# Kernel tuning notes

Hardware: AMD Instinct MI355X
Metric: run time of the kernel (lower is better)

The kernel has to match this reference:

```python
import jax, jax.numpy as jnp
import numpy as np

B, S, D_IN = 2, 2048, 2048
NUM_HEADS, NUM_KV_GROUPS, HEAD_DIM = 32, 8, 64
GROUP_SIZE = NUM_HEADS // NUM_KV_GROUPS  # 4
D_OUT = NUM_HEADS * HEAD_DIM  # 2048


def setup_inputs() -> dict:
    key = jax.random.key(0)
    k1, k2, k3, k4, k5 = jax.random.split(key, 5)
    scale_in = 1.0 / np.sqrt(D_IN)
    scale_out = 1.0 / np.sqrt(D_OUT)
    return {
        "x": jax.random.normal(k1, (B, S, D_IN), dtype=jnp.float32),
        # Linear weights stored torch-style as (out_features, in_features); y = x @ W.T
        "Wq": jax.random.uniform(k2, (D_OUT, D_IN), minval=-scale_in, maxval=scale_in, dtype=jnp.float32),
        "Wk": jax.random.uniform(k3, (NUM_KV_GROUPS * HEAD_DIM, D_IN), minval=-scale_in, maxval=scale_in, dtype=jnp.float32),
        "Wv": jax.random.uniform(k4, (NUM_KV_GROUPS * HEAD_DIM, D_IN), minval=-scale_in, maxval=scale_in, dtype=jnp.float32),
        "Wo": jax.random.uniform(k5, (D_IN, D_OUT), minval=-scale_out, maxval=scale_out, dtype=jnp.float32),
    }


def reference(x, Wq, Wk, Wv, Wo):
    b, s, _ = x.shape
    # Projections
    q = (x @ Wq.T).reshape(b, s, NUM_KV_GROUPS, GROUP_SIZE, HEAD_DIM)  # [b,s,g,r,d]
    k = (x @ Wk.T).reshape(b, s, NUM_KV_GROUPS, HEAD_DIM)              # [b,s,g,d]
    v = (x @ Wv.T).reshape(b, s, NUM_KV_GROUPS, HEAD_DIM)
    # Scores: broadcast each KV group over its group of query heads
    # (equivalent to repeat_interleave of K/V along head dim)
    scores = jnp.einsum("bqgrd,bkgd->bgrqk", q, k) / np.sqrt(HEAD_DIM).astype(jnp.float32)
    causal = jnp.tril(jnp.ones((s, s), dtype=bool))  # True = keep
    scores = jnp.where(causal, scores, jnp.finfo(scores.dtype).min)
    attn = jax.nn.softmax(scores, axis=-1)  # [b,g,r,q,k]
    ctx = jnp.einsum("bgrqk,bkgd->bqgrd", attn, v).reshape(b, s, D_OUT)
    out = ctx @ Wo.T
    # new_kv_cache (un-expanded keys/values, layout [b, g, s, d])
    keys = k.transpose(0, 2, 1, 3)
    values = v.transpose(0, 2, 1, 3)
    return out, (keys, values)
```

## Files before the change

kernel.cpp:

```cpp
#include <hip/hip_runtime.h>


#define B_   2
#define S_   2048
#define DIN  2048
#define NH   32
#define NKV  8
#define HD   64
#define DOUT 2048
#define NQKV 3072

#define QSCALE 0.18033688f

typedef short bf16x8 __attribute__((ext_vector_type(8)));
typedef short bf16x4 __attribute__((ext_vector_type(4)));
typedef float f32x4  __attribute__((ext_vector_type(4)));

__device__ __forceinline__ unsigned short f2bf(float f) {
  unsigned int u = __float_as_uint(f);
  u += 0x7fff + ((u >> 16) & 1);
  return (unsigned short)(u >> 16);
}

__device__ __forceinline__ f32x4 mfma16(bf16x4 a, bf16x4 b, f32x4 c) {
#if __has_builtin(__builtin_amdgcn_mfma_f32_16x16x16bf16_1k)
  return __builtin_amdgcn_mfma_f32_16x16x16bf16_1k(a, b, c, 0, 0, 0);
#else
  asm volatile("v_mfma_f32_16x16x16_bf16 %0, %1, %2, %0" : "+v"(c) : "v"(a), "v"(b));
  return c;
#endif
}

__device__ __forceinline__ void gld_lds16(const void* gptr, void* lptr) {
  __builtin_amdgcn_global_load_lds(
      (const __attribute__((address_space(1))) unsigned int*)gptr,
      (__attribute__((address_space(3))) unsigned int*)lptr,
      16, 0, 0);
}

__device__ __forceinline__ bf16x8 ds_read128(const unsigned short* p) {
  bf16x8 r;
  asm volatile("ds_read_b128 %0, %1"
               : "=v"(r)
               : "v"((const __attribute__((address_space(3))) unsigned short*)p));
  return r;
}

#define BAR() __builtin_amdgcn_s_barrier()
#define SB()  __builtin_amdgcn_sched_barrier(0)
#define VMCNT(n) asm volatile("s_waitcnt vmcnt(" #n ")")
#define LGKM0()                                   \
  do {                                            \
    asm volatile("s_waitcnt lgkmcnt(0)");         \
    __builtin_amdgcn_sched_barrier(0);            \
  } while (0)

__global__ __launch_bounds__(256) void cvt_all(
    const float* __restrict__ x,  const float* __restrict__ Wq,
    const float* __restrict__ Wk, const float* __restrict__ Wv,
    const float* __restrict__ Wo,
    unsigned short* __restrict__ xbf, unsigned short* __restrict__ wqkv,
    unsigned short* __restrict__ wobf) {
  int i = blockIdx.x * blockDim.x + threadIdx.x;
  const float* src; unsigned short* dst; int off;
  if (i < 2097152)      { src = x;  dst = xbf;                  off = i; }
  else if (i < 3145728) { src = Wq; dst = wqkv;                 off = i - 2097152; }
  else if (i < 3407872) { src = Wk; dst = wqkv + 2048 * 2048;   off = i - 3145728; }
  else if (i < 3670016) { src = Wv; dst = wqkv + 2560 * 2048;   off = i - 3407872; }
  else                  { src = Wo; dst = wobf;                 off = i - 3670016; }
  float4 f = ((const float4*)src)[off];
  ushort4 o;
  o.x = f2bf(f.x); o.y = f2bf(f.y); o.z = f2bf(f.z); o.w = f2bf(f.w);
  ((ushort4*)dst)[off] = o;
}

#define MMA_PHASE(MH, NHH, BF)                                                  \
  do {                                                                          \
    __builtin_amdgcn_s_setprio(1);                                              \
    _Pragma("unroll")                                                           \
    for (int kk = 0; kk < 2; ++kk)                                              \
      _Pragma("unroll")                                                         \
      for (int mr = 0; mr < 4; ++mr)                                            \
        _Pragma("unroll")                                                       \
        for (int nr = 0; nr < NR; ++nr)                                         \
          acc[(MH) * 4 + mr][(NHH) * NR + nr] =                                 \
              __builtin_amdgcn_mfma_f32_16x16x32_bf16(                          \
                  af[mr][kk], BF[nr][kk], acc[(MH) * 4 + mr][(NHH) * NR + nr],  \
                  0, 0, 0);                                                     \
    __builtin_amdgcn_s_setprio(0);                                              \
  } while (0)

#define WAITW()                                   \
  do {                                            \
    if constexpr (BN == 256) VMCNT(6);            \
    else                     VMCNT(4);            \
  } while (0)

template <int MODE, int BN, int NTN>
__global__ __launch_bounds__(512, 2) void gemm8p(
    const unsigned short* __restrict__ A,
    const unsigned short* __restrict__ Bm,
    int K,
    unsigned short* __restrict__ qbf,
    unsigned short* __restrict__ kbf,
    unsigned short* __restrict__ vtbf,
    float* __restrict__ kout,
    float* __restrict__ vout,
    float* __restrict__ cout) {
  constexpr int NR = BN / 128;
  constexpr int BHROW = BN / 2;
  __shared__ unsigned short As[2][256 * 64];
  __shared__ unsigned short Bs[2][BN * 64];

  const int tid  = threadIdx.x;
  const int lane = tid & 63;
  const int wave = tid >> 6;
  const int wm   = wave >> 2;
  const int wn   = wave & 3;
  const int quad = lane >> 4;
  const int r16  = lane & 15;

  const int NT = K / 64;

  const int nwg = gridDim.x;
  const int id  = blockIdx.x;
  const int sid = (id & 7) * (nwg >> 3) + (id >> 3);
  const int by  = sid / NTN;
  const int bx  = sid % NTN;
  const int aRowBase = by * 256;
  const int bColBase = bx * BN;

  f32x4 zero = {0.f, 0.f, 0.f, 0.f};
  f32x4 acc[8][2 * NR];
#pragma unroll
  for (int i = 0; i < 8; ++i)
#pragma unroll
    for (int j = 0; j < 2 * NR; ++j) acc[i][j] = zero;

  auto stageA = [&](int dbuf, int h, int t) {
    const int tt = t < NT ? t : NT - 1;
    const int k0 = tt * 64;
#pragma unroll
    for (int i = 0; i < 2; ++i) {
      const int chunk = (i * 8 + wave) * 64 + lane;
      const int row = chunk >> 3;
      const int slot = chunk & 7;
      const int gc = (slot ^ (row & 7)) * 8;
      gld_lds16(A + (size_t)(aRowBase + h * 128 + row) * K + k0 + gc,
                &As[dbuf][h * 8192 + (i * 8 + wave) * 512]);
    }
  };
  auto stageB = [&](int dbuf, int h, int t) {
    const int tt = t < NT ? t : NT - 1;
    const int k0 = tt * 64;
    if constexpr (BN == 256) {
#pragma unroll
      for (int i = 0; i < 2; ++i) {
        const int chunk = (i * 8 + wave) * 64 + lane;
        const int row = chunk >> 3;
        const int slot = chunk & 7;
        const int gc = (slot ^ (row & 7)) * 8;
        gld_lds16(Bm + (size_t)(bColBase + h * 128 + row) * K + k0 + gc,
                  &Bs[dbuf][h * 8192 + (i * 8 + wave) * 512]);
      }
    } else {
      const int chunk = wave * 64 + lane;
      const int row = chunk >> 3;
      const int slot = chunk & 7;
      const int gc = (slot ^ (row & 7)) * 8;
      gld_lds16(Bm + (size_t)(bColBase + h * 64 + row) * K + k0 + gc,
                &Bs[dbuf][h * 4096 + wave * 512]);
    }
  };

  bf16x8 af[4][2];
  bf16x8 b0[NR][2];
  bf16x8 b1[NR][2];

  auto readA = [&](int sbuf, int mh) {
#pragma unroll
    for (int mr = 0; mr < 4; ++mr)
#pragma unroll
      for (int kk = 0; kk < 2; ++kk) {
        const int row = mh * 128 + wm * 64 + mr * 16 + r16;
        const int slot = (kk * 4 + quad) ^ (r16 & 7);
        af[mr][kk] = ds_read128(&As[sbuf][row * 64 + slot * 8]);
      }
  };
  auto readB = [&](int sbuf, int nh, bf16x8 (&bf)[NR][2]) {
#pragma unroll
    for (int nr = 0; nr < NR; ++nr)
#pragma unroll
      for (int kk = 0; kk < 2; ++kk) {
        const int row = nh * BHROW + wn * (BN / 8) + nr * 16 + r16;
        const int slot = (kk * 4 + quad) ^ (r16 & 7);
        bf[nr][kk] = ds_read128(&Bs[sbuf][row * 64 + slot * 8]);
      }
  };

  stageA(0, 0, 0);
  stageB(0, 0, 0);
  stageB(0, 1, 0);
  stageA(0, 1, 0);
  stageA(1, 0, 1);
  stageB(1, 0, 1);
  stageB(1, 1, 1);
  WAITW();
  BAR(); SB();

  const int NIT = NT / 2;
  for (int i = 0; i < NIT; ++i) {
    const int e2 = 2 * i + 2, o2 = 2 * i + 3;

    readA(0, 0); readB(0, 0, b0);
    stageA(1, 1, 2 * i + 1);
    BAR();
    LGKM0();
    MMA_PHASE(0, 0, b0);
    BAR(); SB();

    readB(0, 1, b1);
    stageA(0, 0, e2);
    BAR();
    LGKM0();
    MMA_PHASE(0, 1, b1);
    BAR(); SB();

    readA(0, 1);
    stageB(0, 0, e2);
    BAR();
    LGKM0();
    MMA_PHASE(1, 0, b0);
    BAR(); SB();

    stageB(0, 1, e2);
    BAR();
    MMA_PHASE(1, 1, b1);
    WAITW();
    BAR(); SB();

    readA(1, 0); readB(1, 0, b0);
    stageA(0, 1, e2);
    BAR();
    LGKM0();
    MMA_PHASE(0, 0, b0);
    BAR(); SB();

    readB(1, 1, b1);
    stageA(1, 0, o2);
    BAR();
    LGKM0();
    MMA_PHASE(0, 1, b1);
    BAR(); SB();

    readA(1, 1);
    stageB(1, 0, o2);
    BAR();
    LGKM0();
    MMA_PHASE(1, 0, b0);
    BAR(); SB();

    stageB(1, 1, o2);
    BAR();
    MMA_PHASE(1, 1, b1);
    WAITW();
    BAR(); SB();
  }
  VMCNT(0);

#pragma unroll
  for (int mi = 0; mi < 8; ++mi) {
    const int mh = mi >> 2, mr = mi & 3;
#pragma unroll
    for (int ni = 0; ni < 2 * NR; ++ni) {
      const int nh = ni / NR, nr = ni % NR;
      const int rowb = aRowBase + mh * 128 + wm * 64 + mr * 16 + quad * 4;
      const int col  = bColBase +
                       (BN == 256 ? nh * 128 + wn * 32 + nr * 16
                                  : nh * 64 + wn * 16) + r16;
#pragma unroll
      for (int reg = 0; reg < 4; ++reg) {
        const float v = acc[mi][ni][reg];
        const int m = rowb + reg;
        if (MODE == 1) {
          cout[(size_t)m * DOUT + col] = v;
        } else {
          if (col < 2048) {
            qbf[(size_t)m * DOUT + col] = f2bf(v * QSCALE);
          } else if (col < 2560) {
            const int gg = (col - 2048) >> 6, d = col & 63;
            const int b = m >> 11, s = m & 2047;
            const size_t idx = ((size_t)(b * NKV + gg) * S_ + s) * HD + d;
            kbf[idx]  = f2bf(v);
            kout[idx] = v;
          } else {
            const int gg = (col - 2560) >> 6, d = col & 63;
            const int b = m >> 11, s = m & 2047;
            vtbf[((size_t)(b * NKV + gg) * HD + d) * S_ + s]  = f2bf(v);
            vout[((size_t)(b * NKV + gg) * S_ + s) * HD + d] = v;
          }
        }
      }
    }
  }
}

__global__ __launch_bounds__(512, 4) void attn_kernel(
    const unsigned short* __restrict__ Q,
    const unsigned short* __restrict__ Kb,
    const unsigned short* __restrict__ VT,
    unsigned short* __restrict__ ctx) {
  __shared__ unsigned short Kbuf[2][4096];
  __shared__ unsigned short Vbuf[2][4096];

  const int tid  = threadIdx.x;
  const int lane = tid & 63;
  const int wave = tid >> 6;
  const int grp  = wave >> 2;
  const int hw   = wave & 3;
  const int quad = lane >> 4;
  const int r16  = lane & 15;
  const int g    = blockIdx.y;
  const int b    = blockIdx.z;
  const int h    = g * 4 + hw;
  const int pairI = blockIdx.x;
  const int q0     = grp ? pairI * 32 : (63 - pairI) * 32;
  const int nT_own = grp ? pairI / 2 + 1 : (63 - pairI) / 2 + 1;
  const int nTa    = (63 - pairI) / 2 + 1;

  const unsigned short* Kh  = Kb + (size_t)(b * NKV + g) * S_ * HD;
  const unsigned short* VTh = VT + (size_t)(b * NKV + g) * HD * S_;

  const int srow   = lane >> 3;
  const int schunk = (lane & 7) ^ srow;

  bf16x8 aq[2][2];
#pragma unroll
  for (int mt = 0; mt < 2; ++mt)
#pragma unroll
    for (int kk = 0; kk < 2; ++kk)
      aq[mt][kk] = *(const bf16x8*)(Q + (size_t)(b * S_ + q0 + mt * 16 + r16) * DOUT +
                                    h * HD + kk * 32 + quad * 8);

  bf16x4 ones4;
#pragma unroll
  for (int i = 0; i < 4; ++i) ones4[i] = (short)0x3F80;

  f32x4 zero = {0.f, 0.f, 0.f, 0.f};
  f32x4 o[2][4];
  f32x4 l[2];
#pragma unroll
  for (int mt = 0; mt < 2; ++mt) {
    l[mt] = zero;
#pragma unroll
    for (int dt = 0; dt < 4; ++dt) o[mt][dt] = zero;
  }

  auto stage = [&](int buf, int kt) {
    const int kbase = kt * 64;
    gld_lds16(Kh + (size_t)(kbase + wave * 8 + srow) * HD + schunk * 8,
              &Kbuf[buf][wave * 512]);
    gld_lds16(VTh + (size_t)(wave * 8 + srow) * S_ + kbase + schunk * 8,
              &Vbuf[buf][wave * 512]);
  };

  stage(0, 0);
  __syncthreads();

  for (int kt = 0; kt < nTa; ++kt) {
    const int buf = kt & 1;
    if (kt + 1 < nTa) stage(buf ^ 1, kt + 1);

    if (kt < nT_own) {
      bf16x8 bk[4][2];
#pragma unroll
      for (int nt = 0; nt < 4; ++nt)
#pragma unroll
        for (int kk = 0; kk < 2; ++kk) {
          const int seg = nt * 2 + (r16 >> 3), r = r16 & 7;
          const int slot = (kk * 4 + quad) ^ r;
          bk[nt][kk] = *(const bf16x8*)&Kbuf[buf][seg * 512 + r * 64 + slot * 8];
        }

      const bool last = (kt == nT_own - 1);
#pragma unroll
      for (int mt = 0; mt < 2; ++mt) {
        f32x4 st[4];
#pragma unroll
        for (int nt = 0; nt < 4; ++nt) st[nt] = zero;
#pragma unroll
        for (int kk = 0; kk < 2; ++kk)
#pragma unroll
          for (int nt = 0; nt < 4; ++nt)
            st[nt] = __builtin_amdgcn_mfma_f32_16x16x32_bf16(bk[nt][kk], aq[mt][kk], st[nt], 0, 0, 0);

        bf16x4 pf[4];
#pragma unroll
        for (int nt = 0; nt < 4; ++nt) {
#pragma unroll
          for (int r = 0; r < 4; ++r) {
            float s = st[nt][r];
            if (last) {
              const int key = kt * 64 + nt * 16 + quad * 4 + r;
              const int row = q0 + mt * 16 + r16;
              if (key > row) s = -1e38f;
            }
            const float p = __builtin_amdgcn_exp2f(s);
            pf[nt][r] = (short)(__float_as_uint(p) >> 16);
          }
        }
#pragma unroll
        for (int nt = 0; nt < 4; ++nt) l[mt] = mfma16(pf[nt], ones4, l[mt]);
#pragma unroll
        for (int dt = 0; dt < 4; ++dt) {
          const int seg = dt * 2 + (r16 >> 3), r = r16 & 7;
#pragma unroll
          for (int nt = 0; nt < 4; ++nt) {
            const int slot = (nt * 2 + (quad >> 1)) ^ r;
            bf16x4 bv = *(const bf16x4*)&Vbuf[buf][seg * 512 + r * 64 + slot * 8 + (quad & 1) * 4];
            o[mt][dt] = mfma16(pf[nt], bv, o[mt][dt]);
          }
        }
      }
    }

    __syncthreads();
  }

#pragma unroll
  for (int mt = 0; mt < 2; ++mt) {
    f32x4 rl;
#pragma unroll
    for (int r = 0; r < 4; ++r) rl[r] = __builtin_amdgcn_rcpf(l[mt][r]);
#pragma unroll
    for (int dt = 0; dt < 4; ++dt)
#pragma unroll
      for (int r = 0; r < 4; ++r) {
        const int qq = q0 + mt * 16 + quad * 4 + r;
        ctx[(size_t)(b * S_ + qq) * DOUT + h * HD + dt * 16 + r16] =
            f2bf(o[mt][dt][r] * rl[r]);
      }
  }
}

extern "C" void kernel_launch(void* const* d_in, const int* in_sizes, int n_in,
                              void* d_out, int out_size, void* d_ws, size_t ws_size,
                              hipStream_t stream) {
  const float* x  = (const float*)d_in[0];
  const float* Wq = (const float*)d_in[1];
  const float* Wk = (const float*)d_in[2];
  const float* Wv = (const float*)d_in[3];
  const float* Wo = (const float*)d_in[4];

  float* out  = (float*)d_out;
  float* keys = out + (size_t)B_ * S_ * DOUT;
  float* vals = keys + (size_t)B_ * NKV * S_ * HD;

  unsigned short* xbf  = (unsigned short*)d_ws;
  unsigned short* wqkv = xbf  + (size_t)B_ * S_ * DIN;
  unsigned short* wobf = wqkv + (size_t)NQKV * DIN;
  unsigned short* qbf  = wobf + (size_t)DIN * DOUT;
  unsigned short* kbf  = qbf  + (size_t)B_ * S_ * DOUT;
  unsigned short* vtbf = kbf  + (size_t)B_ * NKV * S_ * HD;
  unsigned short* ctx  = vtbf + (size_t)B_ * NKV * S_ * HD;

  cvt_all<<<dim3(4718592 / 256), dim3(256), 0, stream>>>(x, Wq, Wk, Wv, Wo,
                                                         xbf, wqkv, wobf);

  gemm8p<0, 256, 12><<<dim3(192), dim3(512), 0, stream>>>(
      xbf, wqkv, DIN, qbf, kbf, vtbf, keys, vals, nullptr);

  attn_kernel<<<dim3(32, NKV, B_), dim3(512), 0, stream>>>(qbf, kbf, vtbf, ctx);

  gemm8p<1, 128, 16><<<dim3(256), dim3(512), 0, stream>>>(
      ctx, wobf, DOUT, nullptr, nullptr, nullptr, nullptr, nullptr, out);
}
```

Baseline: 295.6 us.

## Double-buffer A fragments and prefetch LDS reads ahead of MFMA phases

Splits the A-fragment registers into two sets and reorders the GEMM main loop so the LDS reads for the next MFMA phase are issued before the current phase's MFMAs run. This hides LDS read latency behind matrix work instead of waiting on it. The global-load wait points move earlier, with smaller vmcnt thresholds, and the loop prologue now preloads the first fragments. The extra fragment registers raise register pressure under the 512x2 launch bounds, and the retuned barrier and wait placement risks exposing global-load latency.

```diff
diff --git a/kernel.cpp b/kernel.cpp
--- a/kernel.cpp
+++ b/kernel.cpp
@@ -74,7 +74,7 @@
   ((ushort4*)dst)[off] = o;
 }
 
-#define MMA_PHASE(MH, NHH, BF)                                                  \
+#define MMA_PHASE(MH, NHH, AF, BF)                                              \
   do {                                                                          \
     __builtin_amdgcn_s_setprio(1);                                              \
     _Pragma("unroll")                                                           \
@@ -85,15 +85,15 @@
         for (int nr = 0; nr < NR; ++nr)                                         \
           acc[(MH) * 4 + mr][(NHH) * NR + nr] =                                 \
               __builtin_amdgcn_mfma_f32_16x16x32_bf16(                          \
-                  af[mr][kk], BF[nr][kk], acc[(MH) * 4 + mr][(NHH) * NR + nr],  \
+                  AF[mr][kk], BF[nr][kk], acc[(MH) * 4 + mr][(NHH) * NR + nr],  \
                   0, 0, 0);                                                     \
     __builtin_amdgcn_s_setprio(0);                                              \
   } while (0)
 
 #define WAITW()                                   \
   do {                                            \
-    if constexpr (BN == 256) VMCNT(6);            \
-    else                     VMCNT(4);            \
+    if constexpr (BN == 256) VMCNT(4);            \
+    else                     VMCNT(3);            \
   } while (0)
 
 template <int MODE, int BN, int NTN>
@@ -173,28 +173,29 @@
     }
   };
 
-  bf16x8 af[4][2];
+  bf16x8 afA[4][2];
+  bf16x8 afB[4][2];
   bf16x8 b0[NR][2];
   bf16x8 b1[NR][2];
 
-  auto readA = [&](int sbuf, int mh) {
+  auto readA = [&](int sbuf, int mh, bf16x8 (&dst)[4][2]) {
 #pragma unroll
     for (int mr = 0; mr < 4; ++mr)
 #pragma unroll
       for (int kk = 0; kk < 2; ++kk) {
         const int row = mh * 128 + wm * 64 + mr * 16 + r16;
         const int slot = (kk * 4 + quad) ^ (r16 & 7);
-        af[mr][kk] = ds_read128(&As[sbuf][row * 64 + slot * 8]);
+        dst[mr][kk] = ds_read128(&As[sbuf][row * 64 + slot * 8]);
       }
   };
-  auto readB = [&](int sbuf, int nh, bf16x8 (&bf)[NR][2]) {
+  auto readB = [&](int sbuf, int nh, bf16x8 (&dst)[NR][2]) {
 #pragma unroll
     for (int nr = 0; nr < NR; ++nr)
 #pragma unroll
       for (int kk = 0; kk < 2; ++kk) {
         const int row = nh * BHROW + wn * (BN / 8) + nr * 16 + r16;
         const int slot = (kk * 4 + quad) ^ (r16 & 7);
-        bf[nr][kk] = ds_read128(&Bs[sbuf][row * 64 + slot * 8]);
+        dst[nr][kk] = ds_read128(&Bs[sbuf][row * 64 + slot * 8]);
       }
   };
 
@@ -204,69 +205,74 @@
   stageA(0, 1, 0);
   stageA(1, 0, 1);
   stageB(1, 0, 1);
+  WAITW();
+  BAR();
   stageB(1, 1, 1);
-  WAITW();
-  BAR(); SB();
+  readA(0, 0, afA);
+  readB(0, 0, b0);
+  SB();
 
   const int NIT = NT / 2;
   for (int i = 0; i < NIT; ++i) {
     const int e2 = 2 * i + 2, o2 = 2 * i + 3;
 
-    readA(0, 0); readB(0, 0, b0);
     stageA(1, 1, 2 * i + 1);
     BAR();
     LGKM0();
-    MMA_PHASE(0, 0, b0);
-    BAR(); SB();
-
-    readB(0, 1, b1);
+    readB(0, 1, b1); SB();
+    MMA_PHASE(0, 0, afA, b0);
+    BAR();
+
     stageA(0, 0, e2);
     BAR();
     LGKM0();
-    MMA_PHASE(0, 1, b1);
-    BAR(); SB();
-
-    readA(0, 1);
+    readA(0, 1, afB); SB();
+    MMA_PHASE(0, 1, afA, b1);
+    BAR();
+
     stageB(0, 0, e2);
     BAR();
     LGKM0();
-    MMA_PHASE(1, 0, b0);
-    BAR(); SB();
+    MMA_PHASE(1, 0, afB, b0);
+    WAITW();
+    BAR();
 
     stageB(0, 1, e2);
     BAR();
-    MMA_PHASE(1, 1, b1);
+    readA(1, 0, afA);
+    readB(1, 0, b0); SB();
+    MMA_PHASE(1, 1, afB, b1);
+    BAR();
+
+    stageA(0, 1, e2);
+    BAR();
+    LGKM0();
+    readB(1, 1, b1); SB();
+    MMA_PHASE(0, 0, afA, b0);
+    BAR();
+
+    stageA(1, 0, o2);
+    BAR();
+    LGKM0();
+    readA(1, 1, afB); SB();
+    MMA_PHASE(0, 1, afA, b1);
+    BAR();
+
+    stageB(1, 0, o2);
+    BAR();
+    LGKM0();
+    MMA_PHASE(1, 0, afB, b0);
     WAITW();
-    BAR(); SB();
-
-    readA(1, 0); readB(1, 0, b0);
-    stageA(0, 1, e2);
-    BAR();
-    LGKM0();
-    MMA_PHASE(0, 0, b0);
-    BAR(); SB();
-
-    readB(1, 1, b1);
-    stageA(1, 0, o2);
-    BAR();
-    LGKM0();
-    MMA_PHASE(0, 1, b1);
-    BAR(); SB();
-
-    readA(1, 1);
-    stageB(1, 0, o2);
-    BAR();
-    LGKM0();
-    MMA_PHASE(1, 0, b0);
-    BAR(); SB();
+    BAR();
 
     stageB(1, 1, o2);
     BAR();
-    MMA_PHASE(1, 1, b1);
-    WAITW();
-    BAR(); SB();
+    readA(0, 0, afA);
+    readB(0, 0, b0); SB();
+    MMA_PHASE(1, 1, afB, b1);
+    BAR();
   }
-  VMCNT(0);
+  asm volatile("s_waitcnt vmcnt(0) lgkmcnt(0)");
 
 #pragma unroll
   for (int mi = 0; mi < 8; ++mi) {
```

Result: no change. 290.6 us (median of 2 runs) (-1.7%).
